# Performance work log

Hardware: AMD Instinct MI355X
Metric: run time of the kernel (lower is better)

## Reference

```python
import jax, jax.numpy as jnp
import numpy as np

EPS = 1e-12
TEMP = 0.05
LAMBDA2 = 0.5


def _normalize(x):
    # F.normalize(x, dim=1), eps=1e-12
    n = jnp.linalg.norm(x, axis=1, keepdims=True)
    return x / jnp.maximum(n, EPS)


def _cdist(x, f):
    # torch.cdist p=2: [B, N] euclidean distances
    x2 = jnp.sum(x * x, axis=1, keepdims=True)          # [B,1]
    f2 = jnp.sum(f * f, axis=1)[None, :]                # [1,N]
    d2 = x2 + f2 - 2.0 * (x @ f.T)
    return jnp.sqrt(jnp.maximum(d2, 0.0))


def _ce(logits, targets):
    # F.cross_entropy with integer targets, mean reduction
    logp = jax.nn.log_softmax(logits, axis=1)
    return -jnp.take_along_axis(logp, targets[:, None], axis=1).mean()


def _branch_loss(x_raw, f, targets):
    x = _normalize(x_raw)
    # note: original applies cross_entropy (which does another log_softmax)
    # on top of softmax(cdist(...)) -- reproduced faithfully
    soft = jax.nn.softmax(_cdist(x, f), axis=1)
    out = (x @ f.T) / TEMP
    return _ce(out, targets) + _ce(soft, targets)


def setup_inputs() -> dict:
    key = jax.random.key(0)
    ks = jax.random.split(key, 7)
    B, N, D = 256, 8192, 2048
    inputs = jax.random.normal(ks[0], (B, D), dtype=jnp.float32)
    inputs_up = jax.random.normal(ks[1], (B, D), dtype=jnp.float32)
    inputs_down = jax.random.normal(ks[2], (B, D), dtype=jnp.float32)
    targets = jax.random.randint(ks[3], (B,), 0, N)
    # memory banks are buffers; initialize as L2-normalized rows (realistic state)
    features = _normalize(jax.random.normal(ks[4], (N, D), dtype=jnp.float32))
    features_up = _normalize(jax.random.normal(ks[5], (N, D), dtype=jnp.float32))
    features_down = _normalize(jax.random.normal(ks[6], (N, D), dtype=jnp.float32))
    return {
        "inputs": inputs,
        "inputs_up": inputs_up,
        "inputs_down": inputs_down,
        "targets": targets,
        "epoch": 10,
        "features": features,
        "features_up": features_up,
        "features_down": features_down,
    }


def reference(inputs, inputs_up, inputs_down, targets, epoch, features, features_up, features_down):
    l_mid = _branch_loss(inputs, features, targets)
    l_up = _branch_loss(inputs_up, features_up, targets)
    l_down = _branch_loss(inputs_down, features_down, targets)
    loss = (1.0 - LAMBDA2) * l_mid + LAMBDA2 * (l_up + l_down)
    return loss
```

## Files before the change

kernel.cpp:

```cpp
#include <hip/hip_runtime.h>

typedef float f4v __attribute__((ext_vector_type(4)));
typedef float f32x4 __attribute__((ext_vector_type(4)));
typedef __bf16 bf16x8 __attribute__((ext_vector_type(8)));
typedef __bf16 bf16x4 __attribute__((ext_vector_type(4)));
typedef unsigned short ushort8 __attribute__((ext_vector_type(8)));

static constexpr int KDIM = 2048;

static constexpr size_t OFF_XN      = 0;
static constexpr size_t OFF_D       = (size_t)3 * 256 * 2048 * 2;
static constexpr size_t OFF_ROWLOSS = OFF_D + (size_t)2 * 3 * 256 * 8192 * 2;

__device__ __forceinline__ unsigned short f2bf(float x) {
  union { float f; unsigned u; } c; c.f = x;
  unsigned r = c.u + 0x7fffu + ((c.u >> 16) & 1u);
  return (unsigned short)(r >> 16);
}

__device__ __forceinline__ float bf2f(unsigned short u) {
  union { unsigned i; float f; } c; c.i = ((unsigned)u) << 16; return c.f;
}

__device__ __forceinline__ void gload_lds16(const void* g, void* l) {
  __builtin_amdgcn_global_load_lds((const __attribute__((address_space(1))) void*)g,
                                   (__attribute__((address_space(3))) void*)l,
                                   16, 0, 0);
}

__device__ __forceinline__ void cvt_store8(char* p, f4v v) {
  bf16x4 o;
  o[0] = (__bf16)v[0]; o[1] = (__bf16)v[1]; o[2] = (__bf16)v[2]; o[3] = (__bf16)v[3];
  *(bf16x4*)p = o;
}

__global__ __launch_bounds__(256) void k_normalize(
    const float* __restrict__ x0, const float* __restrict__ x1, const float* __restrict__ x2,
    unsigned short* __restrict__ xn)
{
  int bid = blockIdx.x;
  int branch = bid >> 8;
  int row = bid & 255;
  const float* src = (branch == 0 ? x0 : (branch == 1 ? x1 : x2)) + (size_t)row * KDIM;
  int tid = threadIdx.x;
  f4v a = *(const f4v*)(src + tid * 8);
  f4v b = *(const f4v*)(src + tid * 8 + 4);
  float s = a[0]*a[0] + a[1]*a[1] + a[2]*a[2] + a[3]*a[3]
          + b[0]*b[0] + b[1]*b[1] + b[2]*b[2] + b[3]*b[3];
  #pragma unroll
  for (int m = 1; m < 64; m <<= 1) s += __shfl_xor(s, m);
  __shared__ float ls[4];
  if ((tid & 63) == 0) ls[tid >> 6] = s;
  __syncthreads();
  float total = ls[0] + ls[1] + ls[2] + ls[3];
  float inv = 1.0f / fmaxf(sqrtf(total), 1e-12f);
  ushort8 u;
  #pragma unroll
  for (int e = 0; e < 4; ++e) u[e]     = f2bf(a[e] * inv);
  #pragma unroll
  for (int e = 0; e < 4; ++e) u[4 + e] = f2bf(b[e] * inv);
  *(ushort8*)(xn + (size_t)bid * KDIM + tid * 8) = u;
}

__global__ __launch_bounds__(512, 4) void k_gemm(
    const unsigned short* __restrict__ xn,
    const float* __restrict__ f0, const float* __restrict__ f1, const float* __restrict__ f2,
    unsigned short* __restrict__ dW)
{
  __shared__ char lds[2 * 24576];

  int bid = blockIdx.x;
  int swz = (bid & 7) * 48 + (bid >> 3);
  int branch = swz >> 7;
  int rem = swz & 127;
  int ntile = rem >> 1;
  int ks = rem & 1;

  const unsigned short* A = xn + (size_t)branch * 256 * KDIM + ks * 1024;
  const float* F = (branch == 0 ? f0 : (branch == 1 ? f1 : f2))
                 + (size_t)ntile * 128 * KDIM + ks * 1024;

  int tid = threadIdx.x;
  int wave = tid >> 6;
  int lane = tid & 63;
  int rcol0 = lane & 15;
  int klane = lane >> 4;
  int wr = wave >> 1;
  int wc = wave & 1;

  const unsigned short* aSrc = A + (size_t)(tid >> 2) * KDIM
                             + (((tid & 3) ^ ((tid >> 3) & 3)) << 3);
  char* aDst = lds + wave * 1024;

#define STAGE_A(kt, buf) do { \
    gload_lds16(aSrc + (kt) * 32, aDst + (buf) * 24576); \
    gload_lds16(aSrc + (size_t)128 * KDIM + (kt) * 32, aDst + (buf) * 24576 + 8192); \
  } while (0)

  const float* bSrc = F + (size_t)(tid >> 3) * KDIM + (tid & 7) * 4;
  f4v bq0, bq1;

#define LOADB_G(kt) do { \
    bq0 = *(const f4v*)(bSrc + (kt) * 32); \
    bq1 = *(const f4v*)(bSrc + (size_t)64 * KDIM + (kt) * 32); \
  } while (0)

  int bOff = 16384 + (tid >> 3) * 64
           + (((((tid & 7) >> 1)) ^ ((tid >> 4) & 3)) << 4) + (tid & 1) * 8;

#define WRITE_B(buf) do { \
    char* wb = lds + (buf) * 24576 + bOff; \
    cvt_store8(wb, bq0); \
    cvt_store8(wb + 4096, bq1); \
  } while (0)

  f32x4 acc[4][4];
  #pragma unroll
  for (int i = 0; i < 4; ++i)
    #pragma unroll
    for (int j = 0; j < 4; ++j)
      #pragma unroll
      for (int q = 0; q < 4; ++q) acc[i][j][q] = 0.0f;

  int sx = (rcol0 >> 1) & 3;
  int ch = ((klane ^ sx) << 4);
  const char* aRd = lds + (wr * 64 + rcol0) * 64;
  const char* bRd = lds + 16384 + (wc * 64 + rcol0) * 64;

#define COMPUTE(buf) do { \
    const char* ra = aRd + (buf) * 24576 + ch; \
    const char* rb = bRd + (buf) * 24576 + ch; \
    bf16x8 a0 = *(const bf16x8*)(ra); \
    bf16x8 a1 = *(const bf16x8*)(ra + 1024); \
    bf16x8 a2 = *(const bf16x8*)(ra + 2048); \
    bf16x8 a3 = *(const bf16x8*)(ra + 3072); \
    _Pragma("unroll") for (int j = 0; j < 4; ++j) { \
      bf16x8 bj = *(const bf16x8*)(rb + j * 1024); \
      acc[0][j] = __builtin_amdgcn_mfma_f32_16x16x32_bf16(a0, bj, acc[0][j], 0, 0, 0); \
      acc[1][j] = __builtin_amdgcn_mfma_f32_16x16x32_bf16(a1, bj, acc[1][j], 0, 0, 0); \
      acc[2][j] = __builtin_amdgcn_mfma_f32_16x16x32_bf16(a2, bj, acc[2][j], 0, 0, 0); \
      acc[3][j] = __builtin_amdgcn_mfma_f32_16x16x32_bf16(a3, bj, acc[3][j], 0, 0, 0); \
    } \
  } while (0)

  LOADB_G(0);
  STAGE_A(0, 0);
  WRITE_B(0);
  __syncthreads();

  for (int kt = 0; kt < 32; ++kt) {
    int cur = kt & 1;
    if (kt < 31) {
      LOADB_G(kt + 1);
      STAGE_A(kt + 1, cur ^ 1);
    }
    COMPUTE(cur);
    if (kt < 31) WRITE_B(cur ^ 1);
    __syncthreads();
  }

#undef STAGE_A
#undef LOADB_G
#undef WRITE_B
#undef COMPUTE

  unsigned short* Dp = dW + ((size_t)(ks * 3 + branch)) * 256 * 8192
                     + (size_t)ntile * 128 + (size_t)wc * 64 + rcol0;
  #pragma unroll
  for (int i = 0; i < 4; ++i) {
    #pragma unroll
    for (int q = 0; q < 4; ++q) {
      int row = wr * 64 + i * 16 + (klane << 2) + q;
      unsigned short* rp = Dp + (size_t)row * 8192;
      #pragma unroll
      for (int j = 0; j < 4; ++j) rp[j * 16] = f2bf(acc[i][j][q]);
    }
  }
}

__global__ __launch_bounds__(256) void k_row(
    const unsigned short* __restrict__ dW,
    const int* __restrict__ targets,
    float* __restrict__ rowloss)
{
  int row = blockIdx.x;
  int tid = threadIdx.x;
  const unsigned short* p0 = dW + (size_t)row * 8192 + tid * 32;
  const unsigned short* p1 = p0 + (size_t)3 * 256 * 8192;
  int tgt = targets[row & 255];
  int cbase = tid * 32;

  float s1 = 0.f, s2 = 0.f, s3 = 0.f, s4 = 0.f, dt = 0.f;
  #pragma unroll
  for (int g = 0; g < 4; ++g) {
    ushort8 u0 = *(const ushort8*)(p0 + g * 8);
    ushort8 u1 = *(const ushort8*)(p1 + g * 8);
    #pragma unroll
    for (int e = 0; e < 8; ++e) {
      float d = bf2f(u0[e]) + bf2f(u1[e]);
      float e1 = __expf(fmaf(20.0f, d, -20.0f));
      float Dv = sqrtf(fmaxf(2.0f - 2.0f * d, 0.0f));
      float e2 = __expf(Dv - 2.0f);
      s1 += e1; s2 += e2;
      float t2 = e2 * e2;
      s3 += t2; s4 += t2 * e2;
      if (cbase + g * 8 + e == tgt) dt = d;
    }
  }
  #pragma unroll
  for (int m = 1; m < 64; m <<= 1) {
    s1 += __shfl_xor(s1, m); s2 += __shfl_xor(s2, m);
    s3 += __shfl_xor(s3, m); s4 += __shfl_xor(s4, m);
    dt += __shfl_xor(dt, m);
  }
  __shared__ float ls[5][4];
  if ((tid & 63) == 0) {
    int w = tid >> 6;
    ls[0][w] = s1; ls[1][w] = s2; ls[2][w] = s3; ls[3][w] = s4; ls[4][w] = dt;
  }
  __syncthreads();
  if (tid == 0) {
    float p1s = ls[0][0] + ls[0][1] + ls[0][2] + ls[0][3];
    float Z1  = ls[1][0] + ls[1][1] + ls[1][2] + ls[1][3];
    float Z2  = ls[2][0] + ls[2][1] + ls[2][2] + ls[2][3];
    float Z3  = ls[3][0] + ls[3][1] + ls[3][2] + ls[3][3];
    float dtv = ls[4][0] + ls[4][1] + ls[4][2] + ls[4][3];
    float CE1 = 20.0f + logf(p1s) - 20.0f * dtv;
    float Dt = sqrtf(fmaxf(2.0f - 2.0f * dtv, 0.0f));
    float St = __expf(Dt - 2.0f) / Z1;
    float sES = 8193.0f + Z2 / (2.0f * Z1 * Z1) + Z3 / (6.0f * Z1 * Z1 * Z1);
    float CE2 = logf(sES) - St;
    rowloss[row] = (CE1 + CE2) * (0.5f / 256.0f);
  }
}

__global__ __launch_bounds__(256) void k_final(const float* __restrict__ rowloss, float* __restrict__ out)
{
  int tid = threadIdx.x;
  float v = rowloss[tid] + rowloss[tid + 256] + rowloss[tid + 512];
  #pragma unroll
  for (int m = 1; m < 64; m <<= 1) v += __shfl_xor(v, m);
  __shared__ float ls[4];
  if ((tid & 63) == 0) ls[tid >> 6] = v;
  __syncthreads();
  if (tid == 0) out[0] = ls[0] + ls[1] + ls[2] + ls[3];
}

extern "C" void kernel_launch(void* const* d_in, const int* in_sizes, int n_in,
                              void* d_out, int out_size, void* d_ws, size_t ws_size,
                              hipStream_t stream) {
  const float* in0 = (const float*)d_in[0];
  const float* in1 = (const float*)d_in[1];
  const float* in2 = (const float*)d_in[2];
  const int* targets = (const int*)d_in[3];
  const float* f0 = (const float*)d_in[5];
  const float* f1 = (const float*)d_in[6];
  const float* f2 = (const float*)d_in[7];

  char* ws = (char*)d_ws;
  unsigned short* xn = (unsigned short*)(ws + OFF_XN);
  unsigned short* dW = (unsigned short*)(ws + OFF_D);
  float* rowloss = (float*)(ws + OFF_ROWLOSS);
  float* out = (float*)d_out;

  k_normalize<<<768, 256, 0, stream>>>(in0, in1, in2, xn);
  k_gemm<<<384, 512, 0, stream>>>(xn, f0, f1, f2, dW);
  k_row<<<768, 256, 0, stream>>>(dW, targets, rowloss);
  k_final<<<1, 256, 0, stream>>>(rowloss, out);
}
```

Before: 62.47 us.

## Halve GEMM N-tile to 64 with 256-thread blocks and doubled grid

Result: slower. 65.62 us (+5.0%).

```diff
diff --git a/kernel.cpp b/kernel.cpp
--- a/kernel.cpp
+++ b/kernel.cpp
@@ -28,10 +28,11 @@
                                    16, 0, 0);
 }
 
-__device__ __forceinline__ void cvt_store8(char* p, f4v v) {
-  bf16x4 o;
-  o[0] = (__bf16)v[0]; o[1] = (__bf16)v[1]; o[2] = (__bf16)v[2]; o[3] = (__bf16)v[3];
-  *(bf16x4*)p = o;
+__device__ __forceinline__ bf16x8 cvt8(f4v lo, f4v hi) {
+  bf16x8 r;
+  r[0] = (__bf16)lo[0]; r[1] = (__bf16)lo[1]; r[2] = (__bf16)lo[2]; r[3] = (__bf16)lo[3];
+  r[4] = (__bf16)hi[0]; r[5] = (__bf16)hi[1]; r[6] = (__bf16)hi[2]; r[7] = (__bf16)hi[3];
+  return r;
 }
 
 __global__ __launch_bounds__(256) void k_normalize(
@@ -62,56 +63,53 @@
   *(ushort8*)(xn + (size_t)bid * KDIM + tid * 8) = u;
 }
 
-__global__ __launch_bounds__(512, 4) void k_gemm(
+__global__ __launch_bounds__(256, 4) void k_gemm(
     const unsigned short* __restrict__ xn,
     const float* __restrict__ f0, const float* __restrict__ f1, const float* __restrict__ f2,
     unsigned short* __restrict__ dW)
 {
-  __shared__ char lds[2 * 24576];
+  __shared__ char lds[2 * 20480];
 
   int bid = blockIdx.x;
-  int swz = (bid & 7) * 48 + (bid >> 3);
-  int branch = swz >> 7;
-  int rem = swz & 127;
+  int swz = (bid & 7) * 96 + (bid >> 3);
+  int branch = swz >> 8;
+  int rem = swz & 255;
   int ntile = rem >> 1;
   int ks = rem & 1;
 
   const unsigned short* A = xn + (size_t)branch * 256 * KDIM + ks * 1024;
   const float* F = (branch == 0 ? f0 : (branch == 1 ? f1 : f2))
-                 + (size_t)ntile * 128 * KDIM + ks * 1024;
+                 + (size_t)ntile * 64 * KDIM + ks * 1024;
 
   int tid = threadIdx.x;
   int wave = tid >> 6;
   int lane = tid & 63;
   int rcol0 = lane & 15;
   int klane = lane >> 4;
-  int wr = wave >> 1;
-  int wc = wave & 1;
 
   const unsigned short* aSrc = A + (size_t)(tid >> 2) * KDIM
                              + (((tid & 3) ^ ((tid >> 3) & 3)) << 3);
   char* aDst = lds + wave * 1024;
 
 #define STAGE_A(kt, buf) do { \
-    gload_lds16(aSrc + (kt) * 32, aDst + (buf) * 24576); \
-    gload_lds16(aSrc + (size_t)128 * KDIM + (kt) * 32, aDst + (buf) * 24576 + 8192); \
-  } while (0)
-
-  const float* bSrc = F + (size_t)(tid >> 3) * KDIM + (tid & 7) * 4;
+    _Pragma("unroll") for (int g = 0; g < 4; ++g) \
+      gload_lds16(aSrc + (size_t)g * 64 * KDIM + (kt) * 32, \
+                  aDst + (buf) * 20480 + g * 4096); \
+  } while (0)
+
+  const float* bSrc = F + (size_t)(tid >> 2) * KDIM + (tid & 3) * 8;
   f4v bq0, bq1;
 
 #define LOADB_G(kt) do { \
     bq0 = *(const f4v*)(bSrc + (kt) * 32); \
-    bq1 = *(const f4v*)(bSrc + (size_t)64 * KDIM + (kt) * 32); \
-  } while (0)
-
-  int bOff = 16384 + (tid >> 3) * 64
-           + (((((tid & 7) >> 1)) ^ ((tid >> 4) & 3)) << 4) + (tid & 1) * 8;
+    bq1 = *(const f4v*)(bSrc + (kt) * 32 + 4); \
+  } while (0)
+
+  int bOff = 16384 + (tid >> 2) * 64
+           + (((tid & 3) ^ ((tid >> 3) & 3)) << 4);
 
 #define WRITE_B(buf) do { \
-    char* wb = lds + (buf) * 24576 + bOff; \
-    cvt_store8(wb, bq0); \
-    cvt_store8(wb + 4096, bq1); \
+    *(bf16x8*)(lds + (buf) * 20480 + bOff) = cvt8(bq0, bq1); \
   } while (0)
 
   f32x4 acc[4][4];
@@ -124,12 +122,12 @@
 
   int sx = (rcol0 >> 1) & 3;
   int ch = ((klane ^ sx) << 4);
-  const char* aRd = lds + (wr * 64 + rcol0) * 64;
-  const char* bRd = lds + 16384 + (wc * 64 + rcol0) * 64;
+  const char* aRd = lds + (wave * 64 + rcol0) * 64 + ch;
+  const char* bRd = lds + 16384 + rcol0 * 64 + ch;
 
 #define COMPUTE(buf) do { \
-    const char* ra = aRd + (buf) * 24576 + ch; \
-    const char* rb = bRd + (buf) * 24576 + ch; \
+    const char* ra = aRd + (buf) * 20480; \
+    const char* rb = bRd + (buf) * 20480; \
     bf16x8 a0 = *(const bf16x8*)(ra); \
     bf16x8 a1 = *(const bf16x8*)(ra + 1024); \
     bf16x8 a2 = *(const bf16x8*)(ra + 2048); \
@@ -165,12 +163,12 @@
 #undef COMPUTE
 
   unsigned short* Dp = dW + ((size_t)(ks * 3 + branch)) * 256 * 8192
-                     + (size_t)ntile * 128 + (size_t)wc * 64 + rcol0;
+                     + (size_t)ntile * 64 + rcol0;
   #pragma unroll
   for (int i = 0; i < 4; ++i) {
     #pragma unroll
     for (int q = 0; q < 4; ++q) {
-      int row = wr * 64 + i * 16 + (klane << 2) + q;
+      int row = wave * 64 + i * 16 + (klane << 2) + q;
       unsigned short* rp = Dp + (size_t)row * 8192;
       #pragma unroll
       for (int j = 0; j < 4; ++j) rp[j * 16] = f2bf(acc[i][j][q]);
@@ -185,8 +183,8 @@
 {
   int row = blockIdx.x;
   int tid = threadIdx.x;
+  const size_t SPLIT = (size_t)3 * 256 * 8192;
   const unsigned short* p0 = dW + (size_t)row * 8192 + tid * 32;
-  const unsigned short* p1 = p0 + (size_t)3 * 256 * 8192;
   int tgt = targets[row & 255];
   int cbase = tid * 32;
 
@@ -194,7 +192,7 @@
   #pragma unroll
   for (int g = 0; g < 4; ++g) {
     ushort8 u0 = *(const ushort8*)(p0 + g * 8);
-    ushort8 u1 = *(const ushort8*)(p1 + g * 8);
+    ushort8 u1 = *(const ushort8*)(p0 + SPLIT + g * 8);
     #pragma unroll
     for (int e = 0; e < 8; ++e) {
       float d = bf2f(u0[e]) + bf2f(u1[e]);
@@ -264,7 +262,7 @@
   float* out = (float*)d_out;
 
   k_normalize<<<768, 256, 0, stream>>>(in0, in1, in2, xn);
-  k_gemm<<<384, 512, 0, stream>>>(xn, f0, f1, f2, dW);
+  k_gemm<<<768, 256, 0, stream>>>(xn, f0, f1, f2, dW);
   k_row<<<768, 256, 0, stream>>>(dW, targets, rowloss);
   k_final<<<1, 256, 0, stream>>>(rowloss, out);
 }
```
